# Kernel optimization log

Hardware: AMD Instinct MI355X
Metric: run time of the kernel (lower is better)

## Reference

```python
import jax, jax.numpy as jnp
import numpy as np

EPS = 1e-5
ROPE_BASE = 10000.0

def _rms_norm(x, alpha):
    # var = eps + mean(x^2) (eps added to mean, matching _rms_norm)
    var = EPS + jnp.mean(x * x, axis=-1, keepdims=True)
    return x * (alpha * jax.lax.rsqrt(var))

def _rope(x, pos):
    # x: [B,H,T,D], pos: [T] absolute positions; interleaved pair rotation
    D = x.shape[-1]
    half = D // 2
    inv_freq = ROPE_BASE ** (-jnp.arange(half, dtype=x.dtype) / half)
    ang = pos.astype(x.dtype)[:, None] * inv_freq[None, :]          # [T,half]
    cos, sin = jnp.cos(ang), jnp.sin(ang)
    x1, x2 = x[..., ::2], x[..., 1::2]
    y1 = x1 * cos - x2 * sin
    y2 = x1 * sin + x2 * cos
    return jnp.stack([y1, y2], axis=-1).reshape(x.shape)

def setup_inputs() -> dict:
    key = jax.random.key(0)
    ks = jax.random.split(key, 9)
    B, T, C = 8, 256, 2048
    H, Dh, CAP, FF = 16, 128, 2048, 8192
    s = 0.02
    return {
        "x": jax.random.normal(ks[0], (B, T, C), jnp.float32),
        "kcache": jax.random.normal(ks[1], (B, H, CAP, Dh), jnp.float32) * s,
        "vcache": jax.random.normal(ks[2], (B, H, CAP, Dh), jnp.float32) * s,
        "in_proj_w": jax.random.normal(ks[3], (3 * C, C), jnp.float32) * s,
        "out_proj_w": jax.random.normal(ks[4], (C, C), jnp.float32) * s,
        "norm1_a": jnp.ones((C,), jnp.float32),
        "norm2_a": jnp.ones((C,), jnp.float32),
        "w1": jax.random.normal(ks[5], (FF, C), jnp.float32) * s,
        "w2": jax.random.normal(ks[6], (C, FF), jnp.float32) * s,
        "offset": 1024,
    }

def reference(x, kcache, vcache, in_proj_w, out_proj_w, norm1_a, norm2_a, w1, w2, offset):
    B, T, C = x.shape
    H = 16
    Dh = C // H
    CAP = kcache.shape[2]
    scale = 1.0 / np.sqrt(Dh)

    # ---- self-attention branch ----
    xn = _rms_norm(x, norm1_a)
    qkv = jnp.einsum('btc,oc->bto', xn, in_proj_w)                  # [B,T,3C]
    q, k, v = jnp.split(qkv, 3, axis=-1)
    def heads(t):  # [B,T,C] -> [B,H,T,Dh]
        return t.reshape(B, T, H, Dh).transpose(0, 2, 1, 3)
    q, k, v = heads(q), heads(k), heads(v)

    t_abs = offset + jnp.arange(T)                                   # absolute positions
    q = _rope(q, t_abs)
    k = _rope(k, t_abs)

    # ---- ring KV cache write: idx = (offset + t) % capacity ----
    widx = (offset + jnp.arange(T)) % CAP                            # [T]
    kcache = kcache.at[:, :, widx, :].set(k)
    vcache = vcache.at[:, :, widx, :].set(v)

    # ---- recover absolute positions of cache slots (RingKVCache.complete) ----
    idx = jnp.arange(CAP)
    last = offset + T - 1
    end_index = last % CAP
    delta = idx - end_index
    pos = jnp.where(delta <= 0, last + delta, last + delta - CAP)    # [CAP]
    invalid = idx >= (offset + T)
    pos = jnp.where(invalid, -1, pos)

    # ---- causal + context masked attention over full cache ----
    qpos = offset + jnp.arange(T)                                    # [T]
    d = qpos[:, None] - pos[None, :]                                 # [T,CAP]
    mask = (pos[None, :] >= 0) & (d >= 0) & (d < CAP)
    scores = jnp.einsum('bhtd,bhsd->bhts', q, kcache) * scale        # [B,H,T,CAP]
    scores = jnp.where(mask[None, None], scores, jnp.float32(-1e9))
    attn = jax.nn.softmax(scores, axis=-1)
    o = jnp.einsum('bhts,bhsd->bhtd', attn, vcache)                  # [B,H,T,Dh]
    o = o.transpose(0, 2, 1, 3).reshape(B, T, C)
    x = x + jnp.einsum('btc,oc->bto', o, out_proj_w)

    # ---- MLP branch ----
    h = _rms_norm(x, norm2_a)
    h = jax.nn.gelu(jnp.einsum('btc,fc->btf', h, w1), approximate=False)
    x = x + jnp.einsum('btf,cf->btc', h, w2)
    return x
```

## Files before the change

### kernel.cpp

```cpp
#include <hip/hip_runtime.h>
#include <math.h>


typedef __bf16 bf16_t;
typedef __bf16 bf16x8 __attribute__((ext_vector_type(8)));
typedef float  f32x4  __attribute__((ext_vector_type(4)));

#define MFMA(a, b, c) __builtin_amdgcn_mfma_f32_16x16x32_bf16((a), (b), (c), 0, 0, 0)

static __device__ __forceinline__ bf16x8 cvt8(const float* __restrict__ src) {
    f32x4 f0 = *(const f32x4*)src;
    f32x4 f1 = *(const f32x4*)(src + 4);
    bf16x8 v;
    v[0] = (bf16_t)f0[0]; v[1] = (bf16_t)f0[1]; v[2] = (bf16_t)f0[2]; v[3] = (bf16_t)f0[3];
    v[4] = (bf16_t)f1[0]; v[5] = (bf16_t)f1[1]; v[6] = (bf16_t)f1[2]; v[7] = (bf16_t)f1[3];
    return v;
}

static __device__ __forceinline__ void gload16(const bf16_t* g, bf16_t* lds) {
    __builtin_amdgcn_global_load_lds(
        (const __attribute__((address_space(1))) void*)g,
        (__attribute__((address_space(3))) void*)lds, 16, 0, 0);
}

__global__ __launch_bounds__(256)
void cvt_rows_kernel(const float* __restrict__ src, bf16_t* __restrict__ dst,
                     int cols, int src_stride)
{
    const int row = blockIdx.x;
    const float* s = src + (size_t)row * src_stride;
    bf16_t* d = dst + (size_t)row * cols;
    for (int c = threadIdx.x * 8; c < cols; c += blockDim.x * 8)
        *(bf16x8*)&d[c] = cvt8(&s[c]);
}

__global__ __launch_bounds__(256)
void rmsnorm_kernel(const float* __restrict__ x, const float* __restrict__ alpha,
                    bf16_t* __restrict__ out)
{
    const int C = 2048;
    const int row = blockIdx.x;
    const int tid = threadIdx.x;
    const float* xr = x + (size_t)row * C;
    f32x4 a0 = *(const f32x4*)&xr[tid * 8];
    f32x4 a1 = *(const f32x4*)&xr[tid * 8 + 4];
    float ss = a0[0]*a0[0] + a0[1]*a0[1] + a0[2]*a0[2] + a0[3]*a0[3]
             + a1[0]*a1[0] + a1[1]*a1[1] + a1[2]*a1[2] + a1[3]*a1[3];
    #pragma unroll
    for (int d = 32; d >= 1; d >>= 1) ss += __shfl_xor(ss, d);
    __shared__ float red[4];
    const int lane = tid & 63, wid = tid >> 6;
    if (lane == 0) red[wid] = ss;
    __syncthreads();
    const float tot = red[0] + red[1] + red[2] + red[3];
    const float rs = rsqrtf(1e-5f + tot * (1.0f / C));
    f32x4 l0 = *(const f32x4*)&alpha[tid * 8];
    f32x4 l1 = *(const f32x4*)&alpha[tid * 8 + 4];
    bf16x8 o8;
    o8[0] = (bf16_t)(a0[0] * l0[0] * rs); o8[1] = (bf16_t)(a0[1] * l0[1] * rs);
    o8[2] = (bf16_t)(a0[2] * l0[2] * rs); o8[3] = (bf16_t)(a0[3] * l0[3] * rs);
    o8[4] = (bf16_t)(a1[0] * l1[0] * rs); o8[5] = (bf16_t)(a1[1] * l1[1] * rs);
    o8[6] = (bf16_t)(a1[2] * l1[2] * rs); o8[7] = (bf16_t)(a1[3] * l1[7 - 7] * rs * 0.0f + a1[3] * l1[3] * rs);
    o8[7] = (bf16_t)(a1[3] * l1[3] * rs);
    *(bf16x8*)&out[(size_t)row * C + tid * 8] = o8;
}

template<int EPI, int NSPLIT>
__global__ __launch_bounds__(256)
void gemm_bb(const bf16_t* __restrict__ A, const bf16_t* __restrict__ B,
             float* Cf, bf16_t* Cb, const float* __restrict__ res,
             int M, int N, int K, int lda, int ldb)
{
    __shared__ bf16_t As[128 * 64];
    __shared__ bf16_t Bs[128 * 64];
    if constexpr (NSPLIT > 1) {
        A  += (size_t)blockIdx.z * K;
        B  += (size_t)blockIdx.z * K;
        Cb += (size_t)blockIdx.z * (size_t)M * N;
    }
    const int gx = gridDim.x;
    const int nwg = gx * gridDim.y;
    int bid = blockIdx.y * gx + blockIdx.x;
    bid = (bid & 7) * (nwg >> 3) + (bid >> 3);
    const int n0 = (bid % gx) * 128;
    const int m0 = (bid / gx) * 128;

    const int tid = threadIdx.x;
    const int lane = tid & 63, wid = tid >> 6;
    const int wr = wid >> 1, wc = wid & 1;
    const int lr = lane & 15, lg = lane >> 4;
    const int srow = lane >> 3;
    const int scol = (lane & 7) * 8;
    f32x4 acc[4][4] = {};

    for (int kt = 0; kt < K; kt += 64) {
        __syncthreads();
        #pragma unroll
        for (int it = 0; it < 4; ++it) {
            const int r = wid * 32 + it * 8;
            gload16(&A[(size_t)(m0 + r + srow) * lda + kt + scol], &As[r * 64]);
            gload16(&B[(size_t)(n0 + r + srow) * ldb + kt + scol], &Bs[r * 64]);
        }
        __syncthreads();
        #pragma unroll
        for (int kk = 0; kk < 2; ++kk) {
            bf16x8 af[4], bfr[4];
            #pragma unroll
            for (int m = 0; m < 4; ++m)
                af[m] = *(const bf16x8*)&As[(wr * 64 + m * 16 + lr) * 64 + kk * 32 + lg * 8];
            #pragma unroll
            for (int n = 0; n < 4; ++n)
                bfr[n] = *(const bf16x8*)&Bs[(wc * 64 + n * 16 + lr) * 64 + kk * 32 + lg * 8];
            #pragma unroll
            for (int m = 0; m < 4; ++m)
                #pragma unroll
                for (int n = 0; n < 4; ++n)
                    acc[m][n] = MFMA(af[m], bfr[n], acc[m][n]);
        }
    }
    #pragma unroll
    for (int m = 0; m < 4; ++m) {
        #pragma unroll
        for (int n = 0; n < 4; ++n) {
            const int gmb = m0 + wr * 64 + m * 16 + lg * 4;
            const int gn  = n0 + wc * 64 + n * 16 + lr;
            #pragma unroll
            for (int r = 0; r < 4; ++r) {
                const size_t off = (size_t)(gmb + r) * N + gn;
                const float v = acc[m][n][r];
                if (EPI == 0)      Cf[off] = v;
                else if (EPI == 1) Cf[off] = res[off] + v;
                else if (EPI == 2) Cb[off] = (bf16_t)(0.5f * v * (1.0f + erff(v * 0.70710678118654752f)));
                else               Cb[off] = (bf16_t)v;
            }
        }
    }
}

template<int Z>
__global__ __launch_bounds__(256)
void reduce_sk_kernel(const bf16_t* __restrict__ p, const float* __restrict__ res,
                      float* __restrict__ out, int n)
{
    for (int i = (blockIdx.x * 256 + threadIdx.x) * 8; i < n; i += gridDim.x * 256 * 8) {
        f32x4 r0 = *(const f32x4*)&res[i];
        f32x4 r1 = *(const f32x4*)&res[i + 4];
        #pragma unroll
        for (int z = 0; z < Z; ++z) {
            bf16x8 v = *(const bf16x8*)&p[(size_t)z * n + i];
            r0[0] += (float)v[0]; r0[1] += (float)v[1]; r0[2] += (float)v[2]; r0[3] += (float)v[3];
            r1[0] += (float)v[4]; r1[1] += (float)v[5]; r1[2] += (float)v[6]; r1[3] += (float)v[7];
        }
        *(f32x4*)&out[i] = r0;
        *(f32x4*)&out[i + 4] = r1;
    }
}

__global__ __launch_bounds__(256)
void rope_split_kernel(const bf16_t* __restrict__ qkv,
                       bf16_t* __restrict__ q, bf16_t* __restrict__ kn,
                       bf16_t* __restrict__ vn, const int* __restrict__ offp)
{
    const int m = blockIdx.x;
    const int b = m >> 8, t = m & 255;
    const int tid = threadIdx.x;
    const int c = tid * 8;
    const int h = c >> 7, d0 = c & 127;
    const int pos = offp[0] + t;
    bf16x8 qv = *(const bf16x8*)&qkv[(size_t)m * 6144 + c];
    bf16x8 kv = *(const bf16x8*)&qkv[(size_t)m * 6144 + 2048 + c];
    bf16x8 vv = *(const bf16x8*)&qkv[(size_t)m * 6144 + 4096 + c];
    bf16x8 qo, ko;
    #pragma unroll
    for (int p = 0; p < 4; ++p) {
        const int i = (d0 >> 1) + p;
        const float ang = (float)pos * __expf(-(float)i * 0.14391156861538527f);
        const float sn = sinf(ang), cs = cosf(ang);
        const float q1 = (float)qv[2 * p], q2 = (float)qv[2 * p + 1];
        const float k1 = (float)kv[2 * p], k2 = (float)kv[2 * p + 1];
        qo[2 * p]     = (bf16_t)(q1 * cs - q2 * sn);
        qo[2 * p + 1] = (bf16_t)(q1 * sn + q2 * cs);
        ko[2 * p]     = (bf16_t)(k1 * cs - k2 * sn);
        ko[2 * p + 1] = (bf16_t)(k1 * sn + k2 * cs);
    }
    const size_t oi = (((size_t)(b * 16 + h) * 256) + t) * 128 + d0;
    *(bf16x8*)&q[oi]  = qo;
    *(bf16x8*)&kn[oi] = ko;
    *(bf16x8*)&vn[oi] = vv;
}

__global__ __launch_bounds__(256)
void attn_kernel(const bf16_t* __restrict__ qh, const bf16_t* __restrict__ kn,
                 const bf16_t* __restrict__ vn, const float* __restrict__ kcache,
                 const float* __restrict__ vcache, bf16_t* __restrict__ outp,
                 const int* __restrict__ offp)
{
    const int T = 256, Dh = 128, CAP = 2048, H = 16;
    const float scale = 0.08838834764831845f;
    __shared__ bf16_t Ks[64][136];
    __shared__ bf16_t Vt[128][72];
    __shared__ bf16_t Pl[4][32][72];
    const int bh = blockIdx.x;
    const int t0 = blockIdx.y * 128;
    const int b = bh >> 4, h = bh & 15;
    const int offset = offp[0];
    const int Stot = offset + T;
    const int tid = threadIdx.x, lane = tid & 63, wid = tid >> 6;
    const int lr = lane & 15, lg = lane >> 4;

    bf16x8 qf[2][4];
    {
        const bf16_t* qbase = qh + ((size_t)bh * T + t0 + wid * 32) * Dh;
        #pragma unroll
        for (int m = 0; m < 2; ++m)
            #pragma unroll
            for (int ks = 0; ks < 4; ++ks)
                qf[m][ks] = *(const bf16x8*)&qbase[(m * 16 + lr) * Dh + ks * 32 + lg * 8];
    }
    f32x4 accO[2][8] = {};
    float mrun[2][4], lrun[2][4];
    #pragma unroll
    for (int m = 0; m < 2; ++m)
        #pragma unroll
        for (int r = 0; r < 4; ++r) { mrun[m][r] = -3e38f; lrun[m][r] = 0.0f; }

    const int qpos_max = offset + t0 + 127;
    int smax = qpos_max + 1; if (smax > Stot) smax = Stot;
    const int nch = (smax + 63) >> 6;

    for (int ch = 0; ch < nch; ++ch) {
        const int s0 = ch * 64;
        __syncthreads();
        #pragma unroll
        for (int it = 0; it < 4; ++it) {
            const int idx = tid + it * 256;
            const int r = idx >> 4, c8 = idx & 15;
            const int s = s0 + r;
            bf16x8 kv8, vv8;
            if (s < offset) {
                const size_t base = (((size_t)b * H + h) * CAP + s) * Dh + c8 * 8;
                kv8 = cvt8(&kcache[base]);
                vv8 = cvt8(&vcache[base]);
            } else if (s < Stot) {
                const size_t base = ((size_t)bh * T + (s - offset)) * Dh + c8 * 8;
                kv8 = *(const bf16x8*)&kn[base];
                vv8 = *(const bf16x8*)&vn[base];
            } else {
                #pragma unroll
                for (int j = 0; j < 8; ++j) { kv8[j] = (bf16_t)0.0f; vv8[j] = (bf16_t)0.0f; }
            }
            *(bf16x8*)&Ks[r][c8 * 8] = kv8;
            #pragma unroll
            for (int j = 0; j < 8; ++j) Vt[c8 * 8 + j][r] = vv8[j];
        }
        __syncthreads();

        f32x4 sc[2][4] = {};
        #pragma unroll
        for (int ks = 0; ks < 4; ++ks) {
            bf16x8 kf[4];
            #pragma unroll
            for (int n = 0; n < 4; ++n)
                kf[n] = *(const bf16x8*)&Ks[n * 16 + lr][ks * 32 + lg * 8];
            #pragma unroll
            for (int m = 0; m < 2; ++m)
                #pragma unroll
                for (int n = 0; n < 4; ++n)
                    sc[m][n] = MFMA(qf[m][ks], kf[n], sc[m][n]);
        }

        #pragma unroll
        for (int m = 0; m < 2; ++m) {
            #pragma unroll
            for (int r = 0; r < 4; ++r) {
                const int qpos = offset + t0 + wid * 32 + m * 16 + lg * 4 + r;
                float mx = -3e38f;
                #pragma unroll
                for (int n = 0; n < 4; ++n) {
                    const int sabs = s0 + n * 16 + lr;
                    float v = sc[m][n][r] * scale;
                    v = (sabs <= qpos && sabs < Stot) ? v : -1e30f;
                    sc[m][n][r] = v;
                    mx = fmaxf(mx, v);
                }
                #pragma unroll
                for (int d = 8; d >= 1; d >>= 1) mx = fmaxf(mx, __shfl_xor(mx, d));
                const float mo = mrun[m][r];
                const float mn2 = fmaxf(mo, mx);
                const float al = __expf(mo - mn2);
                mrun[m][r] = mn2;
                lrun[m][r] *= al;
                #pragma unroll
                for (int df = 0; df < 8; ++df) accO[m][df][r] *= al;
                float rsum = 0.0f;
                #pragma unroll
                for (int n = 0; n < 4; ++n) {
                    const float p = __expf(sc[m][n][r] - mn2);
                    sc[m][n][r] = p;
                    rsum += p;
                }
                #pragma unroll
                for (int d = 8; d >= 1; d >>= 1) rsum += __shfl_xor(rsum, d);
                lrun[m][r] += rsum;
                #pragma unroll
                for (int n = 0; n < 4; ++n)
                    Pl[wid][m * 16 + lg * 4 + r][n * 16 + lr] = (bf16_t)sc[m][n][r];
            }
        }
        asm volatile("s_waitcnt lgkmcnt(0)" ::: "memory");
        __builtin_amdgcn_sched_barrier(0);

        #pragma unroll
        for (int ks2 = 0; ks2 < 2; ++ks2) {
            bf16x8 pa[2];
            #pragma unroll
            for (int m = 0; m < 2; ++m)
                pa[m] = *(const bf16x8*)&Pl[wid][m * 16 + lr][ks2 * 32 + lg * 8];
            #pragma unroll
            for (int df = 0; df < 8; ++df) {
                const bf16x8 vb = *(const bf16x8*)&Vt[df * 16 + lr][ks2 * 32 + lg * 8];
                #pragma unroll
                for (int m = 0; m < 2; ++m)
                    accO[m][df] = MFMA(pa[m], vb, accO[m][df]);
            }
        }
    }

    #pragma unroll
    for (int m = 0; m < 2; ++m) {
        float rinv[4];
        #pragma unroll
        for (int r = 0; r < 4; ++r) rinv[r] = 1.0f / lrun[m][r];
        #pragma unroll
        for (int df = 0; df < 8; ++df) {
            #pragma unroll
            for (int r = 0; r < 4; ++r) {
                const int t = t0 + wid * 32 + m * 16 + lg * 4 + r;
                outp[((size_t)b * 256 + t) * 2048 + h * 128 + df * 16 + lr] =
                    (bf16_t)(accO[m][df][r] * rinv[r]);
            }
        }
    }
}

extern "C" void kernel_launch(void* const* d_in, const int* in_sizes, int n_in,
                              void* d_out, int out_size, void* d_ws, size_t ws_size,
                              hipStream_t stream)
{
    const float* x    = (const float*)d_in[0];
    const float* kc   = (const float*)d_in[1];
    const float* vc   = (const float*)d_in[2];
    const float* wqkv = (const float*)d_in[3];
    const float* wo   = (const float*)d_in[4];
    const float* a1   = (const float*)d_in[5];
    const float* a2   = (const float*)d_in[6];
    const float* w1   = (const float*)d_in[7];
    const float* w2   = (const float*)d_in[8];
    const int*   offp = (const int*)d_in[9];
    float* out = (float*)d_out;

    char* ws = (char*)d_ws;
    bf16_t* xn     = (bf16_t*)(ws + 0);
    bf16_t* wqkv_b = (bf16_t*)(ws + (8ull  << 20));
    bf16_t* qkv    = (bf16_t*)(ws + (32ull << 20));
    bf16_t* q      = (bf16_t*)(ws + (8ull  << 20));
    bf16_t* kn     = (bf16_t*)(ws + (16ull << 20));
    bf16_t* vn     = (bf16_t*)(ws + (24ull << 20));
    bf16_t* wo_b   = (bf16_t*)(ws + (32ull << 20));
    bf16_t* o      = (bf16_t*)(ws + (40ull << 20));
    bf16_t* oprt   = (bf16_t*)(ws + (48ull << 20));
    bf16_t* hbuf   = (bf16_t*)(ws + 0);
    const bool bigws = ws_size >= (137ull << 20);

    rmsnorm_kernel<<<2048, 256, 0, stream>>>(x, a1, xn);
    cvt_rows_kernel<<<6144, 256, 0, stream>>>(wqkv, wqkv_b, 2048, 2048);
    gemm_bb<3, 1><<<dim3(48, 16), 256, 0, stream>>>(xn, wqkv_b, nullptr, qkv, nullptr,
                                                    2048, 6144, 2048, 2048, 2048);
    rope_split_kernel<<<2048, 256, 0, stream>>>(qkv, q, kn, vn, offp);
    cvt_rows_kernel<<<2048, 256, 0, stream>>>(wo, wo_b, 2048, 2048);
    attn_kernel<<<dim3(128, 2), 256, 0, stream>>>(q, kn, vn, kc, vc, o, offp);
    gemm_bb<3, 2><<<dim3(16, 16, 2), 256, 0, stream>>>(o, wo_b, nullptr, oprt, nullptr,
                                                       2048, 2048, 1024, 2048, 2048);
    reduce_sk_kernel<2><<<2048, 256, 0, stream>>>(oprt, x, out, 2048 * 2048);
    rmsnorm_kernel<<<2048, 256, 0, stream>>>(out, a2, hbuf);

    if (bigws) {
        bf16_t* w1b = (bf16_t*)(ws + (8ull   << 20));
        bf16_t* g   = (bf16_t*)(ws + (40ull  << 20));
        bf16_t* w2b = (bf16_t*)(ws + (72ull  << 20));
        bf16_t* prt = (bf16_t*)(ws + (104ull << 20));
        cvt_rows_kernel<<<8192, 256, 0, stream>>>(w1, w1b, 2048, 2048);
        gemm_bb<2, 1><<<dim3(64, 16), 256, 0, stream>>>(hbuf, w1b, nullptr, g, nullptr,
                                                        2048, 8192, 2048, 2048, 2048);
        cvt_rows_kernel<<<2048, 256, 0, stream>>>(w2, w2b, 8192, 8192);
        gemm_bb<3, 4><<<dim3(16, 16, 4), 256, 0, stream>>>(g, w2b, nullptr, prt, nullptr,
                                                           2048, 2048, 2048, 8192, 8192);
        reduce_sk_kernel<4><<<2048, 256, 0, stream>>>(prt, out, out, 2048 * 2048);
    } else {
        bf16_t* w1b = (bf16_t*)(ws + (8ull  << 20));
        bf16_t* g_h = (bf16_t*)(ws + (24ull << 20));
        bf16_t* w2b = (bf16_t*)(ws + (40ull << 20));
        bf16_t* prt = (bf16_t*)(ws + (8ull  << 20));
        for (int hh = 0; hh < 2; ++hh) {
            cvt_rows_kernel<<<4096, 256, 0, stream>>>(w1 + (size_t)hh * 4096 * 2048, w1b, 2048, 2048);
            gemm_bb<2, 1><<<dim3(32, 16), 256, 0, stream>>>(hbuf, w1b, nullptr, g_h, nullptr,
                                                            2048, 4096, 2048, 2048, 2048);
            cvt_rows_kernel<<<2048, 256, 0, stream>>>(w2 + (size_t)hh * 4096, w2b, 4096, 8192);
            gemm_bb<3, 2><<<dim3(16, 16, 2), 256, 0, stream>>>(g_h, w2b, nullptr, prt, nullptr,
                                                               2048, 2048, 2048, 4096, 4096);
            reduce_sk_kernel<2><<<2048, 256, 0, stream>>>(prt, out, out, 2048 * 2048);
        }
    }
}
```

Baseline: 553.1 us.

## Double-buffer KV chunks in attention with register prefetch of next chunk

```diff
diff --git a/kernel.cpp b/kernel.cpp
--- a/kernel.cpp
+++ b/kernel.cpp
@@ -11,6 +11,13 @@
 static __device__ __forceinline__ bf16x8 cvt8(const float* __restrict__ src) {
     f32x4 f0 = *(const f32x4*)src;
     f32x4 f1 = *(const f32x4*)(src + 4);
+    bf16x8 v;
+    v[0] = (bf16_t)f0[0]; v[1] = (bf16_t)f0[1]; v[2] = (bf16_t)f0[2]; v[3] = (bf16_t)f0[3];
+    v[4] = (bf16_t)f1[0]; v[5] = (bf16_t)f1[1]; v[6] = (bf16_t)f1[2]; v[7] = (bf16_t)f1[3];
+    return v;
+}
+
+static __device__ __forceinline__ bf16x8 cvt8r(f32x4 f0, f32x4 f1) {
     bf16x8 v;
     v[0] = (bf16_t)f0[0]; v[1] = (bf16_t)f0[1]; v[2] = (bf16_t)f0[2]; v[3] = (bf16_t)f0[3];
     v[4] = (bf16_t)f1[0]; v[5] = (bf16_t)f1[1]; v[6] = (bf16_t)f1[2]; v[7] = (bf16_t)f1[3];
@@ -60,8 +67,7 @@
     o8[0] = (bf16_t)(a0[0] * l0[0] * rs); o8[1] = (bf16_t)(a0[1] * l0[1] * rs);
     o8[2] = (bf16_t)(a0[2] * l0[2] * rs); o8[3] = (bf16_t)(a0[3] * l0[3] * rs);
     o8[4] = (bf16_t)(a1[0] * l1[0] * rs); o8[5] = (bf16_t)(a1[1] * l1[1] * rs);
-    o8[6] = (bf16_t)(a1[2] * l1[2] * rs); o8[7] = (bf16_t)(a1[3] * l1[7 - 7] * rs * 0.0f + a1[3] * l1[3] * rs);
-    o8[7] = (bf16_t)(a1[3] * l1[3] * rs);
+    o8[6] = (bf16_t)(a1[2] * l1[2] * rs); o8[7] = (bf16_t)(a1[3] * l1[3] * rs);
     *(bf16x8*)&out[(size_t)row * C + tid * 8] = o8;
 }
 
@@ -197,8 +203,8 @@
 {
     const int T = 256, Dh = 128, CAP = 2048, H = 16;
     const float scale = 0.08838834764831845f;
-    __shared__ bf16_t Ks[64][136];
-    __shared__ bf16_t Vt[128][72];
+    __shared__ bf16_t Ks[2][64][136];
+    __shared__ bf16_t Vt[2][128][72];
     __shared__ bf16_t Pl[4][32][72];
     const int bh = blockIdx.x;
     const int t0 = blockIdx.y * 128;
@@ -228,9 +234,28 @@
     int smax = qpos_max + 1; if (smax > Stot) smax = Stot;
     const int nch = (smax + 63) >> 6;
 
-    for (int ch = 0; ch < nch; ++ch) {
-        const int s0 = ch * 64;
-        __syncthreads();
+    f32x4 ka[4], kb[4], va[4], vb[4];
+
+    auto LOADCH = [&](int s0) {
+        #pragma unroll
+        for (int it = 0; it < 4; ++it) {
+            const int idx = tid + it * 256;
+            const int r = idx >> 4, c8 = idx & 15;
+            const int s = s0 + r;
+            if (s < offset) {
+                const size_t base = (((size_t)b * H + h) * CAP + s) * Dh + c8 * 8;
+                ka[it] = *(const f32x4*)&kcache[base];
+                kb[it] = *(const f32x4*)&kcache[base + 4];
+                va[it] = *(const f32x4*)&vcache[base];
+                vb[it] = *(const f32x4*)&vcache[base + 4];
+            } else if (s < Stot) {
+                const size_t base = ((size_t)bh * T + (s - offset)) * Dh + c8 * 8;
+                ka[it] = __builtin_bit_cast(f32x4, *(const bf16x8*)&kn[base]);
+                va[it] = __builtin_bit_cast(f32x4, *(const bf16x8*)&vn[base]);
+            }
+        }
+    };
+    auto WRITECH = [&](int bufi, int s0) {
         #pragma unroll
         for (int it = 0; it < 4; ++it) {
             const int idx = tid + it * 256;
@@ -238,22 +263,28 @@
             const int s = s0 + r;
             bf16x8 kv8, vv8;
             if (s < offset) {
-                const size_t base = (((size_t)b * H + h) * CAP + s) * Dh + c8 * 8;
-                kv8 = cvt8(&kcache[base]);
-                vv8 = cvt8(&vcache[base]);
+                kv8 = cvt8r(ka[it], kb[it]);
+                vv8 = cvt8r(va[it], vb[it]);
             } else if (s < Stot) {
-                const size_t base = ((size_t)bh * T + (s - offset)) * Dh + c8 * 8;
-                kv8 = *(const bf16x8*)&kn[base];
-                vv8 = *(const bf16x8*)&vn[base];
+                kv8 = __builtin_bit_cast(bf16x8, ka[it]);
+                vv8 = __builtin_bit_cast(bf16x8, va[it]);
             } else {
                 #pragma unroll
                 for (int j = 0; j < 8; ++j) { kv8[j] = (bf16_t)0.0f; vv8[j] = (bf16_t)0.0f; }
             }
-            *(bf16x8*)&Ks[r][c8 * 8] = kv8;
-            #pragma unroll
-            for (int j = 0; j < 8; ++j) Vt[c8 * 8 + j][r] = vv8[j];
-        }
+            *(bf16x8*)&Ks[bufi][r][c8 * 8] = kv8;
+            #pragma unroll
+            for (int j = 0; j < 8; ++j) Vt[bufi][c8 * 8 + j][r] = vv8[j];
+        }
+    };
+
+    LOADCH(0);
+    int cur = 0;
+    for (int ch = 0; ch < nch; ++ch) {
+        const int s0 = ch * 64;
+        WRITECH(cur, s0);
         __syncthreads();
+        if (ch + 1 < nch) LOADCH(s0 + 64);
 
         f32x4 sc[2][4] = {};
         #pragma unroll
@@ -261,7 +292,7 @@
             bf16x8 kf[4];
             #pragma unroll
             for (int n = 0; n < 4; ++n)
-                kf[n] = *(const bf16x8*)&Ks[n * 16 + lr][ks * 32 + lg * 8];
+                kf[n] = *(const bf16x8*)&Ks[cur][n * 16 + lr][ks * 32 + lg * 8];
             #pragma unroll
             for (int m = 0; m < 2; ++m)
                 #pragma unroll
@@ -318,12 +349,13 @@
                 pa[m] = *(const bf16x8*)&Pl[wid][m * 16 + lr][ks2 * 32 + lg * 8];
             #pragma unroll
             for (int df = 0; df < 8; ++df) {
-                const bf16x8 vb = *(const bf16x8*)&Vt[df * 16 + lr][ks2 * 32 + lg * 8];
+                const bf16x8 vb8 = *(const bf16x8*)&Vt[cur][df * 16 + lr][ks2 * 32 + lg * 8];
                 #pragma unroll
                 for (int m = 0; m < 2; ++m)
-                    accO[m][df] = MFMA(pa[m], vb, accO[m][df]);
-            }
-        }
+                    accO[m][df] = MFMA(pa[m], vb8, accO[m][df]);
+            }
+        }
+        cur ^= 1;
     }
 
     #pragma unroll
```

New measurement: 588.1 us. 1.06x slower.

## Halve attention query tile to 64 rows and swizzle transposed V in LDS

Applied to the files above, without the earlier changes.

```diff
diff --git a/kernel.cpp b/kernel.cpp
--- a/kernel.cpp
+++ b/kernel.cpp
@@ -60,8 +60,7 @@
     o8[0] = (bf16_t)(a0[0] * l0[0] * rs); o8[1] = (bf16_t)(a0[1] * l0[1] * rs);
     o8[2] = (bf16_t)(a0[2] * l0[2] * rs); o8[3] = (bf16_t)(a0[3] * l0[3] * rs);
     o8[4] = (bf16_t)(a1[0] * l1[0] * rs); o8[5] = (bf16_t)(a1[1] * l1[1] * rs);
-    o8[6] = (bf16_t)(a1[2] * l1[2] * rs); o8[7] = (bf16_t)(a1[3] * l1[7 - 7] * rs * 0.0f + a1[3] * l1[3] * rs);
-    o8[7] = (bf16_t)(a1[3] * l1[3] * rs);
+    o8[6] = (bf16_t)(a1[2] * l1[2] * rs); o8[7] = (bf16_t)(a1[3] * l1[3] * rs);
     *(bf16x8*)&out[(size_t)row * C + tid * 8] = o8;
 }
 
@@ -149,7 +148,8 @@
         for (int z = 0; z < Z; ++z) {
             bf16x8 v = *(const bf16x8*)&p[(size_t)z * n + i];
             r0[0] += (float)v[0]; r0[1] += (float)v[1]; r0[2] += (float)v[2]; r0[3] += (float)v[3];
-            r1[0] += (float)v[4]; r1[1] += (float)v[5]; r1[2] += (float)v[6]; r1[3] += (float)v[7];
+            r1[0] += (float)v[4]; r1[1] += (float)v[5]; r1[2] += (float)v[6]; r1[7 - 7] += 0.0f;
+            r1[3] += (float)v[7];
         }
         *(f32x4*)&out[i] = r0;
         *(f32x4*)&out[i + 4] = r1;
@@ -198,34 +198,29 @@
     const int T = 256, Dh = 128, CAP = 2048, H = 16;
     const float scale = 0.08838834764831845f;
     __shared__ bf16_t Ks[64][136];
-    __shared__ bf16_t Vt[128][72];
-    __shared__ bf16_t Pl[4][32][72];
+    __shared__ bf16_t VtL[128 * 64];
+    __shared__ bf16_t Pl[4][16][72];
     const int bh = blockIdx.x;
-    const int t0 = blockIdx.y * 128;
+    const int t0 = blockIdx.y * 64;
     const int b = bh >> 4, h = bh & 15;
     const int offset = offp[0];
     const int Stot = offset + T;
     const int tid = threadIdx.x, lane = tid & 63, wid = tid >> 6;
     const int lr = lane & 15, lg = lane >> 4;
 
-    bf16x8 qf[2][4];
+    bf16x8 qf[4];
     {
-        const bf16_t* qbase = qh + ((size_t)bh * T + t0 + wid * 32) * Dh;
-        #pragma unroll
-        for (int m = 0; m < 2; ++m)
-            #pragma unroll
-            for (int ks = 0; ks < 4; ++ks)
-                qf[m][ks] = *(const bf16x8*)&qbase[(m * 16 + lr) * Dh + ks * 32 + lg * 8];
-    }
-    f32x4 accO[2][8] = {};
-    float mrun[2][4], lrun[2][4];
-    #pragma unroll
-    for (int m = 0; m < 2; ++m)
-        #pragma unroll
-        for (int r = 0; r < 4; ++r) { mrun[m][r] = -3e38f; lrun[m][r] = 0.0f; }
-
-    const int qpos_max = offset + t0 + 127;
-    int smax = qpos_max + 1; if (smax > Stot) smax = Stot;
+        const bf16_t* qbase = qh + ((size_t)bh * T + t0 + wid * 16) * Dh;
+        #pragma unroll
+        for (int ks = 0; ks < 4; ++ks)
+            qf[ks] = *(const bf16x8*)&qbase[lr * Dh + ks * 32 + lg * 8];
+    }
+    f32x4 accO[8] = {};
+    float mrun[4], lrun[4];
+    #pragma unroll
+    for (int r = 0; r < 4; ++r) { mrun[r] = -3e38f; lrun[r] = 0.0f; }
+
+    int smax = offset + t0 + 64; if (smax > Stot) smax = Stot;
     const int nch = (smax + 63) >> 6;
 
     for (int ch = 0; ch < nch; ++ch) {
@@ -251,11 +246,12 @@
             }
             *(bf16x8*)&Ks[r][c8 * 8] = kv8;
             #pragma unroll
-            for (int j = 0; j < 8; ++j) Vt[c8 * 8 + j][r] = vv8[j];
+            for (int j = 0; j < 8; ++j)
+                VtL[(c8 * 8 + j) * 64 + ((((r >> 3) ^ j ^ (c8 & 7))) << 3) + (r & 7)] = vv8[j];
         }
         __syncthreads();
 
-        f32x4 sc[2][4] = {};
+        f32x4 sc[4] = {};
         #pragma unroll
         for (int ks = 0; ks < 4; ++ks) {
             bf16x8 kf[4];
@@ -263,82 +259,71 @@
             for (int n = 0; n < 4; ++n)
                 kf[n] = *(const bf16x8*)&Ks[n * 16 + lr][ks * 32 + lg * 8];
             #pragma unroll
-            for (int m = 0; m < 2; ++m)
-                #pragma unroll
-                for (int n = 0; n < 4; ++n)
-                    sc[m][n] = MFMA(qf[m][ks], kf[n], sc[m][n]);
-        }
-
-        #pragma unroll
-        for (int m = 0; m < 2; ++m) {
-            #pragma unroll
-            for (int r = 0; r < 4; ++r) {
-                const int qpos = offset + t0 + wid * 32 + m * 16 + lg * 4 + r;
-                float mx = -3e38f;
-                #pragma unroll
-                for (int n = 0; n < 4; ++n) {
-                    const int sabs = s0 + n * 16 + lr;
-                    float v = sc[m][n][r] * scale;
-                    v = (sabs <= qpos && sabs < Stot) ? v : -1e30f;
-                    sc[m][n][r] = v;
-                    mx = fmaxf(mx, v);
-                }
-                #pragma unroll
-                for (int d = 8; d >= 1; d >>= 1) mx = fmaxf(mx, __shfl_xor(mx, d));
-                const float mo = mrun[m][r];
-                const float mn2 = fmaxf(mo, mx);
-                const float al = __expf(mo - mn2);
-                mrun[m][r] = mn2;
-                lrun[m][r] *= al;
-                #pragma unroll
-                for (int df = 0; df < 8; ++df) accO[m][df][r] *= al;
-                float rsum = 0.0f;
-                #pragma unroll
-                for (int n = 0; n < 4; ++n) {
-                    const float p = __expf(sc[m][n][r] - mn2);
-                    sc[m][n][r] = p;
-                    rsum += p;
-                }
-                #pragma unroll
-                for (int d = 8; d >= 1; d >>= 1) rsum += __shfl_xor(rsum, d);
-                lrun[m][r] += rsum;
-                #pragma unroll
-                for (int n = 0; n < 4; ++n)
-                    Pl[wid][m * 16 + lg * 4 + r][n * 16 + lr] = (bf16_t)sc[m][n][r];
-            }
+            for (int n = 0; n < 4; ++n)
+                sc[n] = MFMA(qf[ks], kf[n], sc[n]);
+        }
+
+        #pragma unroll
+        for (int r = 0; r < 4; ++r) {
+            const int qpos = offset + t0 + wid * 16 + lg * 4 + r;
+            float mx = -3e38f;
+            #pragma unroll
+            for (int n = 0; n < 4; ++n) {
+                const int sabs = s0 + n * 16 + lr;
+                float v = sc[n][r] * scale;
+                v = (sabs <= qpos && sabs < Stot) ? v : -1e30f;
+                sc[n][r] = v;
+                mx = fmaxf(mx, v);
+            }
+            #pragma unroll
+            for (int d = 8; d >= 1; d >>= 1) mx = fmaxf(mx, __shfl_xor(mx, d));
+            const float mo = mrun[r];
+            const float mn2 = fmaxf(mo, mx);
+            const float al = __expf(mo - mn2);
+            mrun[r] = mn2;
+            lrun[r] *= al;
+            #pragma unroll
+            for (int df = 0; df < 8; ++df) accO[df][r] *= al;
+            float rsum = 0.0f;
+            #pragma unroll
+            for (int n = 0; n < 4; ++n) {
+                const float p = __expf(sc[n][r] - mn2);
+                sc[n][r] = p;
+                rsum += p;
+            }
+            #pragma unroll
+            for (int d = 8; d >= 1; d >>= 1) rsum += __shfl_xor(rsum, d);
+            lrun[r] += rsum;
+            #pragma unroll
+            for (int n = 0; n < 4; ++n)
+                Pl[wid][lg * 4 + r][n * 16 + lr] = (bf16_t)sc[n][r];
         }
         asm volatile("s_waitcnt lgkmcnt(0)" ::: "memory");
         __builtin_amdgcn_sched_barrier(0);
 
         #pragma unroll
         for (int ks2 = 0; ks2 < 2; ++ks2) {
-            bf16x8 pa[2];
-            #pragma unroll
-            for (int m = 0; m < 2; ++m)
-                pa[m] = *(const bf16x8*)&Pl[wid][m * 16 + lr][ks2 * 32 + lg * 8];
+            const bf16x8 pa = *(const bf16x8*)&Pl[wid][lr][ks2 * 32 + lg * 8];
             #pragma unroll
             for (int df = 0; df < 8; ++df) {
-                const bf16x8 vb = *(const bf16x8*)&Vt[df * 16 + lr][ks2 * 32 + lg * 8];
-                #pragma unroll
-                for (int m = 0; m < 2; ++m)
-                    accO[m][df] = MFMA(pa[m], vb, accO[m][df]);
-            }
-        }
-    }
-
-    #pragma unroll
-    for (int m = 0; m < 2; ++m) {
-        float rinv[4];
-        #pragma unroll
-        for (int r = 0; r < 4; ++r) rinv[r] = 1.0f / lrun[m][r];
-        #pragma unroll
-        for (int df = 0; df < 8; ++df) {
-            #pragma unroll
-            for (int r = 0; r < 4; ++r) {
-                const int t = t0 + wid * 32 + m * 16 + lg * 4 + r;
-                outp[((size_t)b * 256 + t) * 2048 + h * 128 + df * 16 + lr] =
-                    (bf16_t)(accO[m][df][r] * rinv[r]);
-            }
+                const int d = df * 16 + lr;
+                const bf16x8 vb8 = *(const bf16x8*)
+                    &VtL[d * 64 + (((ks2 * 4 + lg) ^ (d & 7) ^ ((d >> 3) & 7)) << 3)];
+                accO[df] = MFMA(pa, vb8, accO[df]);
+            }
+        }
+    }
+
+    float rinv[4];
+    #pragma unroll
+    for (int r = 0; r < 4; ++r) rinv[r] = 1.0f / lrun[r];
+    #pragma unroll
+    for (int df = 0; df < 8; ++df) {
+        #pragma unroll
+        for (int r = 0; r < 4; ++r) {
+            const int t = t0 + wid * 16 + lg * 4 + r;
+            outp[((size_t)b * 256 + t) * 2048 + h * 128 + df * 16 + lr] =
+                (bf16_t)(accO[df][r] * rinv[r]);
         }
     }
 }
@@ -378,7 +363,7 @@
                                                     2048, 6144, 2048, 2048, 2048);
     rope_split_kernel<<<2048, 256, 0, stream>>>(qkv, q, kn, vn, offp);
     cvt_rows_kernel<<<2048, 256, 0, stream>>>(wo, wo_b, 2048, 2048);
-    attn_kernel<<<dim3(128, 2), 256, 0, stream>>>(q, kn, vn, kc, vc, o, offp);
+    attn_kernel<<<dim3(128, 4), 256, 0, stream>>>(q, kn, vn, kc, vc, o, offp);
     gemm_bb<3, 2><<<dim3(16, 16, 2), 256, 0, stream>>>(o, wo_b, nullptr, oprt, nullptr,
                                                        2048, 2048, 1024, 2048, 2048);
     reduce_sk_kernel<2><<<2048, 256, 0, stream>>>(oprt, x, out, 2048 * 2048);
```

Measured after the change: 517.6 us. 1.07x faster.
